# Kernel tuning notes

Hardware: AMD Instinct MI355X
Metric: run time of the kernel (lower is better)

## Reference

```python
import jax, jax.numpy as jnp
import numpy as np

FRAMES, RANK = 128, 5          # rank=5 implied by create_adj6 non_adj index lists (max index 4)
N = FRAMES * RANK              # 640 nodes
B, NFEAT, NHID, NCLASS = 128, 256, 8, 16
ALPHA = 0.2                    # LeakyReLU negative slope
MASK_VAL = -9e15               # hard mask value from the torch code


def create_adj6(frames, rank):
    """Block-diagonal (with holes) + chain adjacency, exactly as in the torch source."""
    adj = np.zeros((frames * rank, frames * rank), dtype=np.float32)
    non_adj_x = [0, 0, 1, 2, 3, 3, 4, 4]
    non_adj_y = [3, 4, 4, 3, 0, 2, 0, 1]
    for i in range(frames):
        adj[rank * i:rank * (i + 1), rank * i:rank * (i + 1)] = 1
        for j in range(len(non_adj_x)):
            adj[rank * i + non_adj_x[j], rank * i + non_adj_y[j]] = 0
        for j in range(rank):
            if i > 0:
                adj[rank * i + j, rank * (i - 1) + j] = 1
            if i < frames - 1:
                adj[rank * i + j, rank * (i + 1) + j] = 1
    return adj


def _xavier(key, shape):
    fan_in, fan_out = shape[0], shape[1]
    std = np.sqrt(2.0) * np.sqrt(2.0 / (fan_in + fan_out))  # gain=sqrt(2) xavier_normal
    return std * jax.random.normal(key, shape, dtype=jnp.float32)


def setup_inputs() -> dict:
    key = jax.random.key(0)
    ks = jax.random.split(key, 7)
    x = jax.random.normal(ks[0], (B, N, NFEAT), dtype=jnp.float32)
    W1 = _xavier(ks[1], (NFEAT, NHID))
    a11 = _xavier(ks[2], (NHID, 1))
    a12 = _xavier(ks[3], (NHID, 1))
    W2 = _xavier(ks[4], (NHID, NCLASS))  # nhid*nheads=8 -> nclass=16
    a21 = _xavier(ks[5], (NCLASS, 1))
    a22 = _xavier(ks[6], (NCLASS, 1))
    adj = jnp.asarray(create_adj6(FRAMES, RANK) > 0)  # bool [N, N]
    return dict(x=x, W1=W1, a11=a11, a12=a12, W2=W2, a21=a21, a22=a22, adj=adj)


def gat_layer(xi, adj, W, a1, a2):
    # xi: [N, F_in]
    h = xi @ W                              # [N, F_out]
    f1 = h @ a1                             # [N, 1]
    f2 = h @ a2                             # [N, 1]
    e = jax.nn.leaky_relu(f1 + f2.T, negative_slope=ALPHA)  # [N, N]
    scores = jnp.where(adj, e, jnp.float32(MASK_VAL))        # hard additive-style mask
    att = jax.nn.softmax(scores, axis=-1)   # dropout disabled (eval mode)
    return att @ h                          # [N, F_out]


def reference(x, W1, a11, a12, W2, a21, a22, adj):
    def single(xi):
        h1 = gat_layer(xi, adj, W1, a11, a12)          # concat=False -> no elu inside layer
        h2 = jax.nn.elu(gat_layer(h1, adj, W2, a21, a22))
        return jax.nn.log_softmax(h2, axis=1)          # [N, NCLASS]
    return jax.vmap(single)(x)                          # [B, N, NCLASS]
```

## Files before the change

kernel.cpp:

```cpp
#include <hip/hip_runtime.h>

#define B_ 128
#define N_ 640
#define NFEAT 256
#define NHID 8
#define NCLASS 16
#define RANK 5
#define FRAMES 128
#define ALPHA 0.2f
#define PACKMASK 30236135u

#define QSPLIT 8
#define TFRAMES (FRAMES / QSPLIT)
#define TCOUNT (TFRAMES * RANK)
#define BLOCKT 256
#define MAXSTAGE 100
#define H1S 9
#define H2S 17

#define OFF_F1S (MAXSTAGE * H1S)
#define OFF_F2S (OFF_F1S + MAXSTAGE)
#define OFF_HPART (OFF_F2S + MAXSTAGE)
#define OFF_G1S (MAXSTAGE * H2S)
#define OFF_G2S (OFF_G1S + MAXSTAGE)
#define SMEMF (OFF_HPART + MAXSTAGE * H1S)

__device__ __forceinline__ float lrelu(float v) { return v >= 0.0f ? v : ALPHA * v; }

__global__ void __launch_bounds__(BLOCKT, 4) k_fused(
    const float* __restrict__ x, const float* __restrict__ W1,
    const float* __restrict__ a11, const float* __restrict__ a12,
    const float* __restrict__ W2, const float* __restrict__ a21, const float* __restrict__ a22,
    float* __restrict__ out)
{
    __shared__ float smem[SMEMF];
    float* h1s = smem;
    float* f1s = smem + OFF_F1S;
    float* f2s = smem + OFF_F2S;
    float* h2s = smem;
    float* g1s = smem + OFF_G1S;
    float* g2s = smem + OFF_G2S;

    const int bid = blockIdx.x;
    const int bq  = (bid & 7) * 128 + (bid >> 3);
    const int b   = bq >> 3;
    const int q   = bq & 7;

    const int tf_lo  = q * TFRAMES;
    const int l1f_lo = max(tf_lo - 1, 0);
    const int l1f_hi = min(tf_lo + TFRAMES, FRAMES - 1);
    const int stf_lo = max(tf_lo - 2, 0);
    const int stf_hi = min(tf_lo + TFRAMES + 1, FRAMES - 1);
    const int stage_lo  = stf_lo * RANK;
    const int stage_cnt = (stf_hi - stf_lo + 1) * RANK;
    const int l1_lo  = l1f_lo * RANK;
    const int l1_cnt = (l1f_hi - l1f_lo + 1) * RANK;
    const int t_lo   = tf_lo * RANK;

    const int tid  = threadIdx.x;
    const int half = tid >> 7;
    const int r    = tid & 127;

    float h[NHID];
#pragma unroll
    for (int k = 0; k < NHID; ++k) h[k] = 0.0f;

    if (r < stage_cnt) {
        const float* xr = x + ((size_t)b * N_ + stage_lo + r) * NFEAT + (half << 7);
        const float* wb = W1 + (__builtin_amdgcn_readfirstlane(half) << 10);

        float4 xv[16];
#pragma unroll
        for (int c = 0; c < 16; ++c)
            xv[c] = *reinterpret_cast<const float4*>(xr + 4 * c);
#pragma unroll
        for (int c = 0; c < 16; ++c) {
            const float* wq = wb + (c << 5);
#pragma unroll
            for (int k = 0; k < NHID; ++k) {
                h[k] = fmaf(xv[c].x, wq[k], h[k]);
                h[k] = fmaf(xv[c].y, wq[8 + k], h[k]);
                h[k] = fmaf(xv[c].z, wq[16 + k], h[k]);
                h[k] = fmaf(xv[c].w, wq[24 + k], h[k]);
            }
        }
#pragma unroll
        for (int c = 0; c < 16; ++c)
            xv[c] = *reinterpret_cast<const float4*>(xr + 64 + 4 * c);
#pragma unroll
        for (int c = 0; c < 16; ++c) {
            const float* wq = wb + 512 + (c << 5);
#pragma unroll
            for (int k = 0; k < NHID; ++k) {
                h[k] = fmaf(xv[c].x, wq[k], h[k]);
                h[k] = fmaf(xv[c].y, wq[8 + k], h[k]);
                h[k] = fmaf(xv[c].z, wq[16 + k], h[k]);
                h[k] = fmaf(xv[c].w, wq[24 + k], h[k]);
            }
        }
        if (half) {
#pragma unroll
            for (int k = 0; k < NHID; ++k) smem[OFF_HPART + r * H1S + k] = h[k];
        }
    }
    __syncthreads();

    if (tid < stage_cnt) {
        float s1 = 0.0f, s2 = 0.0f;
#pragma unroll
        for (int k = 0; k < NHID; ++k) {
            const float v = h[k] + smem[OFF_HPART + tid * H1S + k];
            s1 = fmaf(v, a11[k], s1);
            s2 = fmaf(v, a12[k], s2);
            h1s[tid * H1S + k] = v;
        }
        f1s[tid] = s1;
        f2s[tid] = s2;
    }
    __syncthreads();

    float h2[NCLASS];
    float s1g = 0.0f, s2g = 0.0f;
    const bool actL1 = (tid < l1_cnt);
    if (actL1) {
        const int u  = l1_lo + tid;
        const int fr = u / RANK;
        const int ru = u - fr * RANK;
        const unsigned rm = (PACKMASK >> (5 * ru)) & 31u;
        const int loc      = u - stage_lo;
        const int base_loc = fr * RANK - stage_lo;
        const bool hp = (fr > 0), hn = (fr < FRAMES - 1);
        const float fu = f1s[loc];

        float m = -1e30f;
        if (hp) m = fmaxf(m, lrelu(fu + f2s[loc - RANK]));
#pragma unroll
        for (int rv = 0; rv < RANK; ++rv)
            if (rm & (1u << rv)) m = fmaxf(m, lrelu(fu + f2s[base_loc + rv]));
        if (hn) m = fmaxf(m, lrelu(fu + f2s[loc + RANK]));

        float s = 0.0f;
        float o1[NHID];
#pragma unroll
        for (int k = 0; k < NHID; ++k) o1[k] = 0.0f;

        auto acc1 = [&](int vloc) {
            float w = __expf(lrelu(fu + f2s[vloc]) - m);
            s += w;
#pragma unroll
            for (int k = 0; k < NHID; ++k) o1[k] = fmaf(w, h1s[vloc * H1S + k], o1[k]);
        };
        if (hp) acc1(loc - RANK);
#pragma unroll
        for (int rv = 0; rv < RANK; ++rv)
            if (rm & (1u << rv)) acc1(base_loc + rv);
        if (hn) acc1(loc + RANK);

        const float inv = 1.0f / s;
#pragma unroll
        for (int k = 0; k < NHID; ++k) o1[k] *= inv;

#pragma unroll
        for (int c = 0; c < NCLASS; ++c) {
            float t = 0.0f;
#pragma unroll
            for (int k = 0; k < NHID; ++k) t = fmaf(o1[k], W2[k * NCLASS + c], t);
            h2[c] = t;
            s1g = fmaf(t, a21[c], s1g);
            s2g = fmaf(t, a22[c], s2g);
        }
    }
    __syncthreads();

    if (actL1) {
        const int loc = l1_lo + tid - stage_lo;
#pragma unroll
        for (int c = 0; c < NCLASS; ++c) h2s[loc * H2S + c] = h2[c];
        g1s[loc] = s1g;
        g2s[loc] = s2g;
    }
    __syncthreads();

    if (tid < TCOUNT) {
        const int u  = t_lo + tid;
        const int fr = u / RANK;
        const int ru = u - fr * RANK;
        const unsigned rm = (PACKMASK >> (5 * ru)) & 31u;
        const int loc      = u - stage_lo;
        const int base_loc = fr * RANK - stage_lo;
        const bool hp = (fr > 0), hn = (fr < FRAMES - 1);
        const float gu = g1s[loc];

        float m = -1e30f;
        if (hp) m = fmaxf(m, lrelu(gu + g2s[loc - RANK]));
#pragma unroll
        for (int rv = 0; rv < RANK; ++rv)
            if (rm & (1u << rv)) m = fmaxf(m, lrelu(gu + g2s[base_loc + rv]));
        if (hn) m = fmaxf(m, lrelu(gu + g2s[loc + RANK]));

        float s = 0.0f;
        float o2[NCLASS];
#pragma unroll
        for (int c = 0; c < NCLASS; ++c) o2[c] = 0.0f;

        auto acc2 = [&](int vloc) {
            float w = __expf(lrelu(gu + g2s[vloc]) - m);
            s += w;
#pragma unroll
            for (int c = 0; c < NCLASS; ++c) o2[c] = fmaf(w, h2s[vloc * H2S + c], o2[c]);
        };
        if (hp) acc2(loc - RANK);
#pragma unroll
        for (int rv = 0; rv < RANK; ++rv)
            if (rm & (1u << rv)) acc2(base_loc + rv);
        if (hn) acc2(loc + RANK);

        const float inv = 1.0f / s;
#pragma unroll
        for (int c = 0; c < NCLASS; ++c) o2[c] *= inv;

#pragma unroll
        for (int c = 0; c < NCLASS; ++c) o2[c] = (o2[c] > 0.0f) ? o2[c] : __expf(o2[c]) - 1.0f;

        float mm = o2[0];
#pragma unroll
        for (int c = 1; c < NCLASS; ++c) mm = fmaxf(mm, o2[c]);
        float ss = 0.0f;
#pragma unroll
        for (int c = 0; c < NCLASS; ++c) ss += __expf(o2[c] - mm);
        const float ls = mm + __logf(ss);

        float* op = out + ((size_t)b * N_ + u) * NCLASS;
#pragma unroll
        for (int c = 0; c < NCLASS; c += 4)
            *reinterpret_cast<float4*>(op + c) =
                make_float4(o2[c] - ls, o2[c + 1] - ls, o2[c + 2] - ls, o2[c + 3] - ls);
    }
}

extern "C" void kernel_launch(void* const* d_in, const int* in_sizes, int n_in,
                              void* d_out, int out_size, void* d_ws, size_t ws_size,
                              hipStream_t stream)
{
    const float* x   = (const float*)d_in[0];
    const float* W1  = (const float*)d_in[1];
    const float* a11 = (const float*)d_in[2];
    const float* a12 = (const float*)d_in[3];
    const float* W2  = (const float*)d_in[4];
    const float* a21 = (const float*)d_in[5];
    const float* a22 = (const float*)d_in[6];
    float* outp = (float*)d_out;

    k_fused<<<B_ * QSPLIT, BLOCKT, 0, stream>>>(x, W1, a11, a12, W2, a21, a22, outp);
}
```

Before: 28.32 us.

## Split x@W1 into MFMA bf16x3 GEMM kernel feeding separate attention kernel

```diff
diff --git a/kernel.cpp b/kernel.cpp
--- a/kernel.cpp
+++ b/kernel.cpp
@@ -1,4 +1,5 @@
 #include <hip/hip_runtime.h>
+#include <stdint.h>
 
 #define B_ 128
 #define N_ 640
@@ -10,25 +11,131 @@
 #define ALPHA 0.2f
 #define PACKMASK 30236135u
 
+typedef short bf16x8 __attribute__((ext_vector_type(8)));
+typedef float f32x4  __attribute__((ext_vector_type(4)));
+typedef unsigned int u32x4 __attribute__((ext_vector_type(4)));
+
+#define GA_ROWS 64
+#define GA_GRID (B_ * N_ / GA_ROWS)
+
+__device__ __forceinline__ void cvt8(float4 p, float4 q, bf16x8& hi, bf16x8& lo)
+{
+    float v[8] = {p.x, p.y, p.z, p.w, q.x, q.y, q.z, q.w};
+    u32x4 hw, lw;
+#pragma unroll
+    for (int i = 0; i < 4; ++i) {
+        const unsigned ua = __float_as_uint(v[2 * i]);
+        const unsigned ub = __float_as_uint(v[2 * i + 1]);
+        hw[i] = (ua >> 16) | (ub & 0xFFFF0000u);
+        const float la = v[2 * i]     - __uint_as_float(ua & 0xFFFF0000u);
+        const float lb = v[2 * i + 1] - __uint_as_float(ub & 0xFFFF0000u);
+        const unsigned va = __float_as_uint(la), vb = __float_as_uint(lb);
+        lw[i] = ((va + 0x7FFFu + ((va >> 16) & 1u)) >> 16)
+              | ((vb + 0x7FFFu + ((vb >> 16) & 1u)) & 0xFFFF0000u);
+    }
+    hi = __builtin_bit_cast(bf16x8, hw);
+    lo = __builtin_bit_cast(bf16x8, lw);
+}
+
+__global__ void __launch_bounds__(256, 4) k_gemm(
+    const float* __restrict__ x, const float* __restrict__ W1,
+    float* __restrict__ h1ws)
+{
+    __shared__ float xs[2][GA_ROWS * 32];
+    const int tid = threadIdx.x;
+    const int w   = tid >> 6;
+    const int l   = tid & 63;
+    const int rowbase = blockIdx.x * GA_ROWS;
+
+    const int n  = l & 15;
+    const int kg = (l >> 4) << 3;
+    bf16x8 bhi[8], blo[8];
+#pragma unroll
+    for (int ks = 0; ks < 8; ++ks) {
+        u32x4 hw, lw;
+#pragma unroll
+        for (int p = 0; p < 4; ++p) {
+            float wa = 0.0f, wb = 0.0f;
+            if (n < NHID) {
+                const int k0 = ks * 32 + kg + 2 * p;
+                wa = W1[k0 * NHID + n];
+                wb = W1[(k0 + 1) * NHID + n];
+            }
+            const unsigned ua = __float_as_uint(wa), ub = __float_as_uint(wb);
+            hw[p] = (ua >> 16) | (ub & 0xFFFF0000u);
+            const float la = wa - __uint_as_float(ua & 0xFFFF0000u);
+            const float lb = wb - __uint_as_float(ub & 0xFFFF0000u);
+            const unsigned va = __float_as_uint(la), vb = __float_as_uint(lb);
+            lw[p] = ((va + 0x7FFFu + ((va >> 16) & 1u)) >> 16)
+                  | ((vb + 0x7FFFu + ((vb >> 16) & 1u)) & 0xFFFF0000u);
+        }
+        bhi[ks] = __builtin_bit_cast(bf16x8, hw);
+        blo[ks] = __builtin_bit_cast(bf16x8, lw);
+    }
+
+    auto stage = [&](int ks, int buf) {
+#pragma unroll
+        for (int rr = 0; rr < 2; ++rr) {
+            const int r  = rr * 32 + (tid >> 3);
+            const int fo = (tid & 7) * 4;
+            const int ff = fo ^ ((r & 3) << 3);
+            const float* gsrc = x + (size_t)(rowbase + r) * NFEAT + ks * 32 + ff;
+            const float* lbase = &xs[buf][rr * 1024 + w * 256];
+            __builtin_amdgcn_global_load_lds(
+                (const __attribute__((address_space(1))) unsigned int*)(const void*)gsrc,
+                (__attribute__((address_space(3))) unsigned int*)(void*)lbase,
+                16, 0, 0);
+        }
+    };
+
+    const int Rrow = w * 16 + (l & 15);
+    const int gsw  = kg ^ ((Rrow & 3) << 3);
+    const int aoff = Rrow * 32 + gsw;
+
+    f32x4 acc = {0.f, 0.f, 0.f, 0.f};
+    stage(0, 0);
+    __syncthreads();
+
+#pragma unroll
+    for (int ks = 0; ks < 8; ++ks) {
+        const int cur = ks & 1;
+        if (ks < 7) stage(ks + 1, cur ^ 1);
+        const float* ap = &xs[cur][aoff];
+        const float4 p = *reinterpret_cast<const float4*>(ap);
+        const float4 q = *reinterpret_cast<const float4*>(ap + 4);
+        bf16x8 ahi, alo;
+        cvt8(p, q, ahi, alo);
+        acc = __builtin_amdgcn_mfma_f32_16x16x32_bf16(ahi, bhi[ks], acc, 0, 0, 0);
+        acc = __builtin_amdgcn_mfma_f32_16x16x32_bf16(alo, bhi[ks], acc, 0, 0, 0);
+        acc = __builtin_amdgcn_mfma_f32_16x16x32_bf16(ahi, blo[ks], acc, 0, 0, 0);
+        __syncthreads();
+    }
+
+    if (n < NHID) {
+        float* hp = h1ws + ((size_t)rowbase + w * 16 + (l >> 4) * 4) * NHID + n;
+#pragma unroll
+        for (int j = 0; j < 4; ++j) hp[j * NHID] = acc[j];
+    }
+}
+
 #define QSPLIT 8
 #define TFRAMES (FRAMES / QSPLIT)
 #define TCOUNT (TFRAMES * RANK)
-#define BLOCKT 256
+#define BLOCKB 128
 #define MAXSTAGE 100
 #define H1S 9
 #define H2S 17
 
 #define OFF_F1S (MAXSTAGE * H1S)
 #define OFF_F2S (OFF_F1S + MAXSTAGE)
-#define OFF_HPART (OFF_F2S + MAXSTAGE)
 #define OFF_G1S (MAXSTAGE * H2S)
 #define OFF_G2S (OFF_G1S + MAXSTAGE)
-#define SMEMF (OFF_HPART + MAXSTAGE * H1S)
+#define SMEMF (OFF_G2S + MAXSTAGE)
 
 __device__ __forceinline__ float lrelu(float v) { return v >= 0.0f ? v : ALPHA * v; }
 
-__global__ void __launch_bounds__(BLOCKT, 4) k_fused(
-    const float* __restrict__ x, const float* __restrict__ W1,
+__global__ void __launch_bounds__(BLOCKB, 8) k_attn(
+    const float* __restrict__ h1ws,
     const float* __restrict__ a11, const float* __restrict__ a12,
     const float* __restrict__ W2, const float* __restrict__ a21, const float* __restrict__ a22,
     float* __restrict__ out)
@@ -57,62 +164,19 @@
     const int l1_cnt = (l1f_hi - l1f_lo + 1) * RANK;
     const int t_lo   = tf_lo * RANK;
 
-    const int tid  = threadIdx.x;
-    const int half = tid >> 7;
-    const int r    = tid & 127;
-
-    float h[NHID];
-#pragma unroll
-    for (int k = 0; k < NHID; ++k) h[k] = 0.0f;
-
-    if (r < stage_cnt) {
-        const float* xr = x + ((size_t)b * N_ + stage_lo + r) * NFEAT + (half << 7);
-        const float* wb = W1 + (__builtin_amdgcn_readfirstlane(half) << 10);
-
-        float4 xv[16];
-#pragma unroll
-        for (int c = 0; c < 16; ++c)
-            xv[c] = *reinterpret_cast<const float4*>(xr + 4 * c);
-#pragma unroll
-        for (int c = 0; c < 16; ++c) {
-            const float* wq = wb + (c << 5);
-#pragma unroll
-            for (int k = 0; k < NHID; ++k) {
-                h[k] = fmaf(xv[c].x, wq[k], h[k]);
-                h[k] = fmaf(xv[c].y, wq[8 + k], h[k]);
-                h[k] = fmaf(xv[c].z, wq[16 + k], h[k]);
-                h[k] = fmaf(xv[c].w, wq[24 + k], h[k]);
-            }
-        }
-#pragma unroll
-        for (int c = 0; c < 16; ++c)
-            xv[c] = *reinterpret_cast<const float4*>(xr + 64 + 4 * c);
-#pragma unroll
-        for (int c = 0; c < 16; ++c) {
-            const float* wq = wb + 512 + (c << 5);
-#pragma unroll
-            for (int k = 0; k < NHID; ++k) {
-                h[k] = fmaf(xv[c].x, wq[k], h[k]);
-                h[k] = fmaf(xv[c].y, wq[8 + k], h[k]);
-                h[k] = fmaf(xv[c].z, wq[16 + k], h[k]);
-                h[k] = fmaf(xv[c].w, wq[24 + k], h[k]);
-            }
-        }
-        if (half) {
-#pragma unroll
-            for (int k = 0; k < NHID; ++k) smem[OFF_HPART + r * H1S + k] = h[k];
-        }
-    }
-    __syncthreads();
+    const int tid = threadIdx.x;
 
     if (tid < stage_cnt) {
+        const float* hp = h1ws + ((size_t)b * N_ + stage_lo + tid) * NHID;
+        const float4 p = *reinterpret_cast<const float4*>(hp);
+        const float4 q4 = *reinterpret_cast<const float4*>(hp + 4);
+        float hv[NHID] = {p.x, p.y, p.z, p.w, q4.x, q4.y, q4.z, q4.w};
         float s1 = 0.0f, s2 = 0.0f;
 #pragma unroll
         for (int k = 0; k < NHID; ++k) {
-            const float v = h[k] + smem[OFF_HPART + tid * H1S + k];
-            s1 = fmaf(v, a11[k], s1);
-            s2 = fmaf(v, a12[k], s2);
-            h1s[tid * H1S + k] = v;
+            s1 = fmaf(hv[k], a11[k], s1);
+            s2 = fmaf(hv[k], a12[k], s2);
+            h1s[tid * H1S + k] = hv[k];
         }
         f1s[tid] = s1;
         f2s[tid] = s2;
@@ -249,7 +313,9 @@
     const float* W2  = (const float*)d_in[4];
     const float* a21 = (const float*)d_in[5];
     const float* a22 = (const float*)d_in[6];
-    float* outp = (float*)d_out;
-
-    k_fused<<<B_ * QSPLIT, BLOCKT, 0, stream>>>(x, W1, a11, a12, W2, a21, a22, outp);
+    float* outp  = (float*)d_out;
+    float* h1ws  = (float*)d_ws;
+
+    k_gemm<<<GA_GRID, 256, 0, stream>>>(x, W1, h1ws);
+    k_attn<<<B_ * QSPLIT, BLOCKB, 0, stream>>>(h1ws, a11, a12, W2, a21, a22, outp);
 }
```

After: 28.77 us. About the same (+1.6%).
